# Performance work log

Measured on AMD Instinct MI355X. Metric: run time of the kernel, lower is better.

The kernel has to match this reference:

```python
import jax, jax.numpy as jnp
import numpy as np

B, NUM_IN = 256, 4096
C1, C2 = 64, 128
K1, K2, P1, P2 = 9, 5, 4, 2
POOL1, POOL2 = 4, 4
H = 256            # rnn_hidden_size
H1, H2 = 256, 128  # mlp hidden sizes
EPS = 1e-5


def setup_inputs() -> dict:
    key = jax.random.key(0)
    ks = jax.random.split(key, 24)
    g = lambda k, shp, scale=0.02: (jax.random.normal(k, shp, jnp.float32) * scale)
    return {
        "x": jax.random.normal(ks[0], (B, 1, NUM_IN), jnp.float32),
        "s": jax.random.normal(ks[1], (B, 1), jnp.float32),
        "conv1_w": g(ks[2], (C1, 1, K1), 0.1), "conv1_b": g(ks[3], (C1,)),
        "bn1_g": jnp.ones((C1,), jnp.float32), "bn1_b": jnp.zeros((C1,), jnp.float32),
        "conv2_w": g(ks[4], (C2, C1, K2), 0.05), "conv2_b": g(ks[5], (C2,)),
        "bn2_g": jnp.ones((C2,), jnp.float32), "bn2_b": jnp.zeros((C2,), jnp.float32),
        "lstm_wi0": g(ks[6], (C2, 4 * H), 0.05), "lstm_bi0": g(ks[7], (4 * H,)),
        "lstm_wh0": g(ks[8], (H, 4 * H), 0.05), "lstm_bh0": g(ks[9], (4 * H,)),
        "lstm_wi1": g(ks[10], (H, 4 * H), 0.05), "lstm_bi1": g(ks[11], (4 * H,)),
        "lstm_wh1": g(ks[12], (H, 4 * H), 0.05), "lstm_bh1": g(ks[13], (4 * H,)),
        "w1": g(ks[14], (H + 1, H1), 0.05), "b1": g(ks[15], (H1,)),
        "w2": g(ks[16], (H1, H2), 0.05), "b2": g(ks[17], (H2,)),
        "wp": g(ks[18], (H2, 1), 0.05), "bp": g(ks[19], (1,)),
    }


def _conv1d(x, w, b, stride, pad):
    # x: [B,C,L], w: [O,I,K]
    y = jax.lax.conv_general_dilated(x, w, (stride,), [(pad, pad)],
                                     dimension_numbers=("NCH", "OIH", "NCH"))
    return y + b[None, :, None]


def _avgpool(x, k):
    Bx, Cx, L = x.shape
    return x.reshape(Bx, Cx, L // k, k).mean(axis=-1)


def _bn(x, gamma, beta):
    # training-mode batchnorm over (N, L) per channel, biased variance
    mu = x.mean(axis=(0, 2), keepdims=True)
    var = ((x - mu) ** 2).mean(axis=(0, 2), keepdims=True)
    xh = (x - mu) * jax.lax.rsqrt(var + EPS)
    return xh * gamma[None, :, None] + beta[None, :, None]


def _lstm_cell(xt, h, c, wi, bi, wh, bh):
    gates = xt @ wi + bi + h @ wh + bh
    i, f, g, o = jnp.split(gates, 4, axis=-1)
    c_new = jax.nn.sigmoid(f) * c + jax.nn.sigmoid(i) * jnp.tanh(g)
    h_new = jax.nn.sigmoid(o) * jnp.tanh(c_new)
    return h_new, c_new


def reference(x, s, conv1_w, conv1_b, bn1_g, bn1_b, conv2_w, conv2_b, bn2_g, bn2_b,
              lstm_wi0, lstm_bi0, lstm_wh0, lstm_bh0,
              lstm_wi1, lstm_bi1, lstm_wh1, lstm_bh1,
              w1, b1, w2, b2, wp, bp):
    x = _bn(_avgpool(jax.nn.relu(_conv1d(x, conv1_w, conv1_b, 1, P1)), POOL1), bn1_g, bn1_b)
    x = _bn(_avgpool(jax.nn.relu(_conv1d(x, conv2_w, conv2_b, 1, P2)), POOL2), bn2_g, bn2_b)
    seq = jnp.transpose(x, (0, 2, 1))          # [B, T, C2]
    seq_t = jnp.transpose(seq, (1, 0, 2))      # [T, B, C2]
    Bx = seq.shape[0]
    init = (jnp.zeros((Bx, H), x.dtype), jnp.zeros((Bx, H), x.dtype),
            jnp.zeros((Bx, H), x.dtype), jnp.zeros((Bx, H), x.dtype))

    def step(carry, xt):
        h0, c0, h1, c1 = carry
        h0, c0 = _lstm_cell(xt, h0, c0, lstm_wi0, lstm_bi0, lstm_wh0, lstm_bh0)
        h1, c1 = _lstm_cell(h0, h1, c1, lstm_wi1, lstm_bi1, lstm_wh1, lstm_bh1)
        return (h0, c0, h1, c1), None

    (h0, c0, h1, c1), _ = jax.lax.scan(step, init, seq_t)
    feat = jnp.concatenate([h1, s], axis=1)    # [B, H+1]
    z = jax.nn.relu(feat @ w1 + b1)            # dropout is identity at eval
    z = jax.nn.relu(z @ w2 + b2)
    return jax.nn.softplus(z @ wp + bp)        # [B, 1]
```

## Files before the change

kernel.cpp:

```cpp
#include <hip/hip_runtime.h>
#include <hip/hip_bf16.h>
#include <hip/hip_fp16.h>
#include <math.h>

#define EPSV 1e-5f

typedef short short8 __attribute__((ext_vector_type(8)));
typedef float f32x4 __attribute__((ext_vector_type(4)));
typedef unsigned long long u64;

#define MFMA(a, b, c) __builtin_amdgcn_mfma_f32_16x16x32_f16(a, b, c, 0, 0, 0)

#define OFF_SC1    8192
#define OFF_SH1    8448
#define OFF_SC2    8704
#define OFF_SH2    9216
#define OFF_B0     9728
#define OFF_B1     13824
#define OFF_PART1  17920
#define OFF_PART2  148992
#define OFF_W2F    411136
#define OFF_WF     493056
#define OFF_SEQ    2328064
#define OFF_H0W    19105280
#define OFF_H1W    19629568
#define OFF_HF     20153856

__device__ __forceinline__ unsigned short f2h(float f) {
  return __half_as_ushort(__float2half(f));
}
__device__ __forceinline__ float h2f(unsigned short u) {
  return __half2float(__ushort_as_half(u));
}
__device__ __forceinline__ float sigf(float x) { return 1.f / (1.f + __expf(-x)); }
__device__ __forceinline__ float tanhfast(float x) {
  return 1.f - 2.f / (__expf(2.f * x) + 1.f);
}

__global__ void k_init(u64* hz) {
  hz[blockIdx.x * 256 + threadIdx.x] = 0ULL;
}

__global__ __launch_bounds__(256, 2) void k_conv1(const float* __restrict__ x,
                                                  const float* __restrict__ w1,
                                                  const float* __restrict__ b1,
                                                  float* __restrict__ part1) {
  __shared__ float xs[4104];
  __shared__ float w1s[576];
  __shared__ float b1s[64];
  __shared__ float red[64][4][2];
  const int tid = threadIdx.x, b = blockIdx.x;
  for (int j = tid; j < 4104; j += 256) {
    int p = j - 4;
    xs[j] = (p >= 0 && p < 4096) ? x[b * 4096 + p] : 0.f;
  }
  for (int j = tid; j < 576; j += 256) w1s[j] = w1[j];
  if (tid < 64) b1s[tid] = b1[tid];
  __syncthreads();
  const int c = tid >> 2, lq = tid & 3;
  float wr[9];
#pragma unroll
  for (int k = 0; k < 9; k++) wr[k] = w1s[c * 9 + k];
  const float bb = b1s[c];
  float S = 0.f, SS = 0.f;
  for (int li = 0; li < 256; li++) {
    int l = lq * 256 + li;
    int base = 4 * l;
    float a4 = 0.f;
#pragma unroll
    for (int jj = 0; jj < 4; jj++) {
      float cv = bb;
#pragma unroll
      for (int k = 0; k < 9; k++) cv += xs[base + jj + k] * wr[k];
      a4 += fmaxf(cv, 0.f);
    }
    float y = 0.25f * a4;
    S += y;
    SS += y * y;
  }
  red[c][lq][0] = S;
  red[c][lq][1] = SS;
  __syncthreads();
  if (tid < 64) {
    float s = 0.f, ss = 0.f;
#pragma unroll
    for (int q = 0; q < 4; q++) {
      s += red[tid][q][0];
      ss += red[tid][q][1];
    }
    part1[(b * 64 + tid) * 2 + 0] = s;
    part1[(b * 64 + tid) * 2 + 1] = ss;
  }
}

__global__ void k_bn1(const float* __restrict__ part1, const float* __restrict__ g,
                      const float* __restrict__ bt, float* __restrict__ sc,
                      float* __restrict__ sh) {
  __shared__ float rs[256], rss[256];
  const int c = blockIdx.x, tid = threadIdx.x;
  rs[tid] = part1[(tid * 64 + c) * 2 + 0];
  rss[tid] = part1[(tid * 64 + c) * 2 + 1];
  __syncthreads();
  for (int st = 128; st > 0; st >>= 1) {
    if (tid < st) {
      rs[tid] += rs[tid + st];
      rss[tid] += rss[tid + st];
    }
    __syncthreads();
  }
  if (tid == 0) {
    const float N = 256.f * 1024.f;
    float mean = rs[0] / N;
    float var = rss[0] / N - mean * mean;
    float scale = g[c] * rsqrtf(var + EPSV);
    sc[c] = scale;
    sh[c] = bt[c] - mean * scale;
  }
}

__global__ void k_w2frag(const float* __restrict__ w2,
                         unsigned short* __restrict__ w2f) {
  int n = blockIdx.x * 256 + threadIdx.x;
  if (n >= 40960) return;
  int e = n & 7, lane = (n >> 3) & 63, ot = (n >> 9) & 7, sc = n >> 12;
  int s = sc >> 1, c2 = sc & 1;
  int o = ot * 16 + (lane & 15);
  int i = c2 * 32 + ((lane >> 4) << 3) + e;
  w2f[n] = f2h(w2[o * 320 + i * 5 + s]);
}

__global__ __launch_bounds__(256, 1) void k_conv2(
    const float* __restrict__ x, const float* __restrict__ w1,
    const float* __restrict__ b1, const float* __restrict__ sc1,
    const float* __restrict__ sh1, const unsigned short* __restrict__ w2f,
    const float* __restrict__ b2, unsigned short* __restrict__ seq,
    float* __restrict__ part2) {
  __shared__ float xs[4104];
  __shared__ unsigned short y1t[1028][66];
  __shared__ float w1s[576], b1s[64], s1s[64], h1s[64], b2s[128];
  __shared__ float red[4][2][128];
  const int tid = threadIdx.x, b = blockIdx.x;
  for (int j = tid; j < 4104; j += 256) {
    int p = j - 4;
    xs[j] = (p >= 0 && p < 4096) ? x[b * 4096 + p] : 0.f;
  }
  for (int j = tid; j < 576; j += 256) w1s[j] = w1[j];
  if (tid < 64) {
    b1s[tid] = b1[tid];
    s1s[tid] = sc1[tid];
    h1s[tid] = sh1[tid];
  }
  if (tid < 128) b2s[tid] = b2[tid];
  if (tid < 132) {
    int r4 = tid / 33, c4 = tid % 33;
    int row = (r4 < 2) ? r4 : (1024 + r4);
    ((unsigned int*)&y1t[row][0])[c4] = 0u;
  }
  __syncthreads();
  {
    const int i2 = tid & 31, lg = tid >> 5;
    const int ia = 2 * i2, ib = ia + 1;
    float wra[9], wrb[9];
#pragma unroll
    for (int k = 0; k < 9; k++) {
      wra[k] = w1s[ia * 9 + k];
      wrb[k] = w1s[ib * 9 + k];
    }
    const float bia = b1s[ia], bib = b1s[ib];
    const float sa = s1s[ia], sb = s1s[ib], ha = h1s[ia], hb = h1s[ib];
    for (int j = 0; j < 128; j++) {
      int l = lg * 128 + j;
      float xv[12];
#pragma unroll
      for (int m = 0; m < 12; m++) xv[m] = xs[4 * l + m];
      float aa = 0.f, ab = 0.f;
#pragma unroll
      for (int jj = 0; jj < 4; jj++) {
        float ca = bia, cb = bib;
#pragma unroll
        for (int k = 0; k < 9; k++) {
          float xx = xv[jj + k];
          ca += xx * wra[k];
          cb += xx * wrb[k];
        }
        aa += fmaxf(ca, 0.f);
        ab += fmaxf(cb, 0.f);
      }
      float va = 0.25f * aa * sa + ha;
      float vb = 0.25f * ab * sb + hb;
      unsigned int pk = (unsigned int)f2h(va) | ((unsigned int)f2h(vb) << 16);
      *(unsigned int*)&y1t[l + 2][ia] = pk;
    }
  }
  __syncthreads();
  const int wv = tid >> 6, lane = tid & 63;
  const int colo = lane & 15, rq = lane >> 4;
  float Sa[2][4], SSa[2][4];
#pragma unroll
  for (int a = 0; a < 2; a++)
#pragma unroll
    for (int c = 0; c < 4; c++) {
      Sa[a][c] = 0.f;
      SSa[a][c] = 0.f;
    }
#pragma unroll
  for (int og = 0; og < 2; og++) {
    short8 bf[4][10];
#pragma unroll
    for (int ot = 0; ot < 4; ot++)
#pragma unroll
      for (int sc = 0; sc < 10; sc++)
        bf[ot][sc] = *(const short8*)(w2f + ((sc * 8 + og * 4 + ot) * 64 + lane) * 8);
    for (int ltw = 0; ltw < 16; ltw++) {
      int lt = wv * 16 + ltw;
      int lbase = lt * 16;
      short8 af[10];
#pragma unroll
      for (int s = 0; s < 5; s++)
#pragma unroll
        for (int c2 = 0; c2 < 2; c2++)
          af[s * 2 + c2] =
              *(const short8*)&y1t[lbase + colo + s][c2 * 32 + rq * 8];
#pragma unroll
      for (int ot = 0; ot < 4; ot++) {
        f32x4 acc = {0.f, 0.f, 0.f, 0.f};
#pragma unroll
        for (int sc = 0; sc < 10; sc++)
          acc = MFMA(af[sc], bf[ot][sc], acc);
        int o = (og * 4 + ot) * 16 + colo;
        float bv = b2s[o];
        float s4 = fmaxf(acc[0] + bv, 0.f) + fmaxf(acc[1] + bv, 0.f) +
                   fmaxf(acc[2] + bv, 0.f) + fmaxf(acc[3] + bv, 0.f);
        float y = 0.25f * s4;
        int t_out = lt * 4 + rq;
        seq[(b * 256 + t_out) * 128 + o] = f2h(y);
        Sa[og][ot] += y;
        SSa[og][ot] += y * y;
      }
    }
  }
#pragma unroll
  for (int og = 0; og < 2; og++)
#pragma unroll
    for (int ot = 0; ot < 4; ot++) {
      float sv = Sa[og][ot], ssv = SSa[og][ot];
      sv += __shfl_xor(sv, 16, 64);
      sv += __shfl_xor(sv, 32, 64);
      ssv += __shfl_xor(ssv, 16, 64);
      ssv += __shfl_xor(ssv, 32, 64);
      if (rq == 0) {
        int o = (og * 4 + ot) * 16 + colo;
        red[wv][0][o] = sv;
        red[wv][1][o] = ssv;
      }
    }
  __syncthreads();
  if (tid < 128) {
    float s = red[0][0][tid] + red[1][0][tid] + red[2][0][tid] + red[3][0][tid];
    float ss = red[0][1][tid] + red[1][1][tid] + red[2][1][tid] + red[3][1][tid];
    part2[(b * 128 + tid) * 2 + 0] = s;
    part2[(b * 128 + tid) * 2 + 1] = ss;
  }
}

__global__ void k_bn2(const float* __restrict__ part2, const float* __restrict__ g,
                      const float* __restrict__ bt, float* __restrict__ sc,
                      float* __restrict__ sh) {
  __shared__ float rs[256], rss[256];
  const int o = blockIdx.x, tid = threadIdx.x;
  rs[tid] = part2[(tid * 128 + o) * 2 + 0];
  rss[tid] = part2[(tid * 128 + o) * 2 + 1];
  __syncthreads();
  for (int st = 128; st > 0; st >>= 1) {
    if (tid < st) {
      rs[tid] += rs[tid + st];
      rss[tid] += rss[tid + st];
    }
    __syncthreads();
  }
  if (tid == 0) {
    const float N = 65536.f;
    float mean = rs[0] / N;
    float var = rss[0] / N - mean * mean;
    float scale = g[o] * rsqrtf(var + EPSV);
    sc[o] = scale;
    sh[o] = bt[o] - mean * scale;
  }
}

__global__ void k_bias(const float* __restrict__ bi0, const float* __restrict__ bh0,
                       const float* __restrict__ wi0, const float* __restrict__ sh2,
                       const float* __restrict__ bi1, const float* __restrict__ bh1,
                       float* __restrict__ b0arr, float* __restrict__ b1arr) {
  int g = blockIdx.x * 256 + threadIdx.x;
  float s = bi0[g] + bh0[g];
  for (int k = 0; k < 128; k++) s += sh2[k] * wi0[k * 1024 + g];
  b0arr[g] = s;
  b1arr[g] = bi1[g] + bh1[g];
}

__global__ void k_wfrag(const float* __restrict__ wi0, const float* __restrict__ wh0,
                        const float* __restrict__ wi1, const float* __restrict__ wh1,
                        const float* __restrict__ sc2,
                        unsigned short* __restrict__ wf) {
  const int slot = blockIdx.x / 56;
  const int idx = (blockIdx.x % 56) * 256 + threadIdx.x;
  const int j = idx >> 9, lane = (idx >> 3) & 63, e = idx & 7;
  const int sh = slot >> 2, wv = slot & 3;
  const int m = lane & 15;
  const int gcol = (m & 3) * 256 + sh * 16 + wv * 4 + (m >> 2);
  float v;
  if (j < 12) {
    int k = j * 32 + ((lane >> 4) << 3) + e;
    v = (k < 128) ? sc2[k] * wi0[k * 1024 + gcol] : wh0[(k - 128) * 1024 + gcol];
  } else {
    int k = (j - 12) * 32 + ((lane >> 4) << 3) + e;
    v = (k < 256) ? wi1[k * 1024 + gcol] : wh1[(k - 256) * 1024 + gcol];
  }
  wf[slot * 14336 + idx] = f2h(v);
}

__global__ __launch_bounds__(256, 1) void k_lstm(
    const unsigned short* __restrict__ seq, const unsigned short* __restrict__ wf,
    const float* __restrict__ b0arr, const float* __restrict__ b1arr,
    u64* __restrict__ h0w, u64* __restrict__ h1w, float* __restrict__ hfinal) {
  __shared__ unsigned short wlds[4 * 28 * 64 * 8];
  __shared__ unsigned short hs0[2][16 * 264];
  __shared__ unsigned short hs1[2][16 * 264];
  const int tid = threadIdx.x;
  const int gb = blockIdx.x >> 4, sh = blockIdx.x & 15;
  const int b0 = gb * 16;
  const int wv = tid >> 6, lane = tid & 63;
  const int bt = lane & 15;
  const int ul = lane >> 4;
  const int q8 = ul * 8;

  {
    const u64* src = (const u64*)(wf + sh * 4 * 14336);
    u64* dst = (u64*)wlds;
    for (int j = tid; j < 14336; j += 256) dst[j] = src[j];
  }
#define LW(j) (*(const short8*)&wlds[(((wv)*28 + (j)) * 64 + lane) * 8])

  f32x4 b0v, b1v;
#pragma unroll
  for (int r = 0; r < 4; r++) {
    int gcol = r * 256 + sh * 16 + wv * 4 + ul;
    b0v[r] = b0arr[gcol];
    b1v[r] = b1arr[gcol];
  }
  float c0 = 0.f, c1 = 0.f, h1v = 0.f;
  const int pidx = (sh * 8 + wv * 2 + (ul >> 1)) * 16 + bt;
  u64* const st0base = h0w + gb * 2048 + pidx;
  u64* const st1base = h1w + gb * 2048 + pidx;
  __syncthreads();

  {
    const unsigned short* xp = seq + ((b0 + bt) * 256 + 0) * 128 + q8;
    short8 xa0 = *(const short8*)(xp + 0);
    short8 xa1 = *(const short8*)(xp + 32);
    short8 xa2 = *(const short8*)(xp + 64);
    short8 xa3 = *(const short8*)(xp + 96);
    f32x4 acc = b0v;
    acc = MFMA(LW(0), xa0, acc);
    acc = MFMA(LW(1), xa1, acc);
    acc = MFMA(LW(2), xa2, acc);
    acc = MFMA(LW(3), xa3, acc);
    c0 = sigf(acc[1]) * c0 + sigf(acc[0]) * tanhfast(acc[2]);
    float h0v = sigf(acc[3]) * tanhfast(c0);
    unsigned v0 = f2h(h0v);
    unsigned v1 = __shfl_down(v0, 16, 64);
    if ((ul & 1) == 0) {
      u64 w = 1ULL | ((u64)v0 << 16) | ((u64)v1 << 32);
      __hip_atomic_store(st0base, w, __ATOMIC_RELAXED, __HIP_MEMORY_SCOPE_AGENT);
    }
  }

  for (int t = 0; t < 256; t++) {
    short8 xa0, xa1, xa2, xa3;
    if (t < 255) {
      const unsigned short* xp = seq + ((b0 + bt) * 256 + (t + 1)) * 128 + q8;
      xa0 = *(const short8*)(xp + 0);
      xa1 = *(const short8*)(xp + 32);
      xa2 = *(const short8*)(xp + 64);
      xa3 = *(const short8*)(xp + 96);
    }
    const u64* q0 = h0w + (t & 1) * 32768 + gb * 2048;
    const u64* q1 = h1w + ((t + 1) & 1) * 32768 + gb * 2048;
    const unsigned e0 = (unsigned)(t + 1), e1 = (unsigned)t;
    u64 w0[8], w1[8];
#pragma unroll
    for (int u = 0; u < 8; u++)
      w1[u] = __hip_atomic_load(q1 + u * 256 + tid, __ATOMIC_RELAXED,
                                __HIP_MEMORY_SCOPE_AGENT);
    {
      int spin = 0;
      for (;;) {
        bool ok = true;
#pragma unroll
        for (int u = 0; u < 8; u++)
          w0[u] = __hip_atomic_load(q0 + u * 256 + tid, __ATOMIC_RELAXED,
                                    __HIP_MEMORY_SCOPE_AGENT);
#pragma unroll
        for (int u = 0; u < 8; u++)
          ok = ok & ((unsigned)(unsigned short)w0[u] == e0);
        if (__all(ok)) break;
        if (++spin > 2) __builtin_amdgcn_s_sleep(2);
      }
    }
    {
      bool ok = true;
#pragma unroll
      for (int u = 0; u < 8; u++)
        ok = ok & ((unsigned)(unsigned short)w1[u] == e1);
      while (!__all(ok)) {
        ok = true;
#pragma unroll
        for (int u = 0; u < 8; u++) {
          w1[u] = __hip_atomic_load(q1 + u * 256 + tid, __ATOMIC_RELAXED,
                                    __HIP_MEMORY_SCOPE_AGENT);
          ok = ok & ((unsigned)(unsigned short)w1[u] == e1);
        }
      }
    }
    const int hb = t & 1;
#pragma unroll
    for (int u = 0; u < 8; u++) {
      int g = u * 256 + tid;
      int bw = g & 15, p = g >> 4;
      *(unsigned*)&hs0[hb][bw * 264 + 2 * p] = (unsigned)(w0[u] >> 16);
      *(unsigned*)&hs1[hb][bw * 264 + 2 * p] = (unsigned)(w1[u] >> 16);
    }
    __syncthreads();
    short8 ha[8], hbf[8];
#pragma unroll
    for (int kk = 0; kk < 8; kk++) {
      ha[kk] = *(const short8*)&hs0[hb][bt * 264 + kk * 32 + q8];
      hbf[kk] = *(const short8*)&hs1[hb][bt * 264 + kk * 32 + q8];
    }
    if (t < 255) {
      f32x4 a0a = b0v;
      f32x4 a0b = {0.f, 0.f, 0.f, 0.f};
      a0a = MFMA(LW(0), xa0, a0a);
      a0b = MFMA(LW(1), xa1, a0b);
      a0a = MFMA(LW(2), xa2, a0a);
      a0b = MFMA(LW(3), xa3, a0b);
#pragma unroll
      for (int kk = 0; kk < 8; kk += 2) {
        a0a = MFMA(LW(4 + kk), ha[kk], a0a);
        a0b = MFMA(LW(5 + kk), ha[kk + 1], a0b);
      }
      float gi = a0a[0] + a0b[0], gf = a0a[1] + a0b[1];
      float gg = a0a[2] + a0b[2], go = a0a[3] + a0b[3];
      c0 = sigf(gf) * c0 + sigf(gi) * tanhfast(gg);
      float h0v = sigf(go) * tanhfast(c0);
      unsigned v0 = f2h(h0v);
      unsigned v1 = __shfl_down(v0, 16, 64);
      if ((ul & 1) == 0) {
        u64 w = (u64)(unsigned short)(t + 2) | ((u64)v0 << 16) | ((u64)v1 << 32);
        __hip_atomic_store(st0base + ((t + 1) & 1) * 32768, w, __ATOMIC_RELAXED,
                           __HIP_MEMORY_SCOPE_AGENT);
      }
    }
    {
      f32x4 acc1a = b1v;
      f32x4 acc1b = {0.f, 0.f, 0.f, 0.f};
#pragma unroll
      for (int kk = 0; kk < 8; kk++) {
        acc1a = MFMA(LW(12 + kk), ha[kk], acc1a);
        acc1b = MFMA(LW(20 + kk), hbf[kk], acc1b);
      }
      float gi = acc1a[0] + acc1b[0], gf = acc1a[1] + acc1b[1];
      float gg = acc1a[2] + acc1b[2], go = acc1a[3] + acc1b[3];
      c1 = sigf(gf) * c1 + sigf(gi) * tanhfast(gg);
      h1v = sigf(go) * tanhfast(c1);
      if (t < 255) {
        unsigned v0 = f2h(h1v);
        unsigned v1 = __shfl_down(v0, 16, 64);
        if ((ul & 1) == 0) {
          u64 w = (u64)(unsigned short)(t + 1) | ((u64)v0 << 16) | ((u64)v1 << 32);
          __hip_atomic_store(st1base + (t & 1) * 32768, w, __ATOMIC_RELAXED,
                             __HIP_MEMORY_SCOPE_AGENT);
        }
      }
    }
  }
  hfinal[(b0 + bt) * 256 + sh * 16 + wv * 4 + ul] = h1v;
}

__global__ __launch_bounds__(256, 2) void k_mlp(const float* __restrict__ hfinal,
                                                const float* __restrict__ s,
                                                const float* __restrict__ w1,
                                                const float* __restrict__ b1,
                                                const float* __restrict__ w2,
                                                const float* __restrict__ b2,
                                                const float* __restrict__ wp,
                                                const float* __restrict__ bp,
                                                float* __restrict__ out) {
  __shared__ float feat[257];
  __shared__ float z1[256];
  __shared__ float z2[128];
  const int tid = threadIdx.x, b = blockIdx.x;
  feat[tid] = hfinal[b * 256 + tid];
  if (tid == 0) feat[256] = s[b];
  __syncthreads();
  float a = b1[tid];
  for (int i = 0; i < 257; i++) a += feat[i] * w1[i * 256 + tid];
  z1[tid] = fmaxf(a, 0.f);
  __syncthreads();
  if (tid < 128) {
    float a2 = b2[tid];
    for (int i = 0; i < 256; i++) a2 += z1[i] * w2[i * 128 + tid];
    z2[tid] = fmaxf(a2, 0.f);
  }
  __syncthreads();
  if (tid == 0) {
    float sv = bp[0];
    for (int i = 0; i < 128; i++) sv += z2[i] * wp[i];
    out[b] = fmaxf(sv, 0.f) + log1pf(__expf(-fabsf(sv)));
  }
}

extern "C" void kernel_launch(void* const* d_in, const int* in_sizes, int n_in,
                              void* d_out, int out_size, void* d_ws, size_t ws_size,
                              hipStream_t stream) {
  const float* x = (const float*)d_in[0];
  const float* s = (const float*)d_in[1];
  const float* c1w = (const float*)d_in[2];
  const float* c1b = (const float*)d_in[3];
  const float* bn1g = (const float*)d_in[4];
  const float* bn1b = (const float*)d_in[5];
  const float* c2w = (const float*)d_in[6];
  const float* c2b = (const float*)d_in[7];
  const float* bn2g = (const float*)d_in[8];
  const float* bn2b = (const float*)d_in[9];
  const float* wi0 = (const float*)d_in[10];
  const float* bi0 = (const float*)d_in[11];
  const float* wh0 = (const float*)d_in[12];
  const float* bh0 = (const float*)d_in[13];
  const float* wi1 = (const float*)d_in[14];
  const float* bi1 = (const float*)d_in[15];
  const float* wh1 = (const float*)d_in[16];
  const float* bh1 = (const float*)d_in[17];
  const float* w1 = (const float*)d_in[18];
  const float* b1 = (const float*)d_in[19];
  const float* w2 = (const float*)d_in[20];
  const float* b2 = (const float*)d_in[21];
  const float* wp = (const float*)d_in[22];
  const float* bp = (const float*)d_in[23];

  char* ws = (char*)d_ws;
  float* sc1 = (float*)(ws + OFF_SC1);
  float* sh1 = (float*)(ws + OFF_SH1);
  float* sc2 = (float*)(ws + OFF_SC2);
  float* sh2 = (float*)(ws + OFF_SH2);
  float* b0arr = (float*)(ws + OFF_B0);
  float* b1arr = (float*)(ws + OFF_B1);
  float* part1 = (float*)(ws + OFF_PART1);
  float* part2 = (float*)(ws + OFF_PART2);
  unsigned short* w2f = (unsigned short*)(ws + OFF_W2F);
  unsigned short* wf = (unsigned short*)(ws + OFF_WF);
  unsigned short* seq = (unsigned short*)(ws + OFF_SEQ);
  u64* h0w = (u64*)(ws + OFF_H0W);
  u64* h1w = (u64*)(ws + OFF_H1W);
  float* hf = (float*)(ws + OFF_HF);

  k_init<<<512, 256, 0, stream>>>(h0w);
  k_conv1<<<256, 256, 0, stream>>>(x, c1w, c1b, part1);
  k_bn1<<<64, 256, 0, stream>>>(part1, bn1g, bn1b, sc1, sh1);
  k_w2frag<<<160, 256, 0, stream>>>(c2w, w2f);
  k_conv2<<<256, 256, 0, stream>>>(x, c1w, c1b, sc1, sh1, w2f, c2b, seq, part2);
  k_bn2<<<128, 256, 0, stream>>>(part2, bn2g, bn2b, sc2, sh2);
  k_bias<<<4, 256, 0, stream>>>(bi0, bh0, wi0, sh2, bi1, bh1, b0arr, b1arr);
  k_wfrag<<<3584, 256, 0, stream>>>(wi0, wh0, wi1, wh1, sc2, wf);
  k_lstm<<<256, 256, 0, stream>>>(seq, wf, b0arr, b1arr, h0w, h1w, hf);
  k_mlp<<<256, 256, 0, stream>>>(hf, s, w1, b1, w2, b2, wp, bp, (float*)d_out);
}
```

Measured before the change: 918.1 us.

## Defer layer-1 hidden-state wait until after input-side MFMAs; triple-buffer h1 exchange

The persistent LSTM kernel now waits only for the layer-0 hidden state at the start of each step. It issues the layer-1 input MFMAs on h0 before spinning on the layer-1 recurrent state, so cross-block sync latency overlaps with compute. The h1 exchange buffer goes from double to triple buffering (mod 3 indexing), with the workspace offset and init size enlarged to match. The cost is an extra __syncthreads per step, modulo arithmetic, and removal of the s_sleep backoff in the h0 spin loop, which can raise memory polling pressure.

Result: slower. 965.0 us (+5.1%).

```diff
diff --git a/kernel.cpp b/kernel.cpp
--- a/kernel.cpp
+++ b/kernel.cpp
@@ -24,7 +24,7 @@
 #define OFF_SEQ    2328064
 #define OFF_H0W    19105280
 #define OFF_H1W    19629568
-#define OFF_HF     20153856
+#define OFF_HF     20416000
 
 __device__ __forceinline__ unsigned short f2h(float f) {
   return __half_as_ushort(__float2half(f));
@@ -38,7 +38,8 @@
 }
 
 __global__ void k_init(u64* hz) {
-  hz[blockIdx.x * 256 + threadIdx.x] = 0ULL;
+  int i = blockIdx.x * 256 + threadIdx.x;
+  if (i < 163840) hz[i] = 0ULL;
 }
 
 __global__ __launch_bounds__(256, 2) void k_conv1(const float* __restrict__ x,
@@ -386,42 +387,20 @@
       xa3 = *(const short8*)(xp + 96);
     }
     const u64* q0 = h0w + (t & 1) * 32768 + gb * 2048;
-    const u64* q1 = h1w + ((t + 1) & 1) * 32768 + gb * 2048;
-    const unsigned e0 = (unsigned)(t + 1), e1 = (unsigned)t;
-    u64 w0[8], w1[8];
-#pragma unroll
-    for (int u = 0; u < 8; u++)
-      w1[u] = __hip_atomic_load(q1 + u * 256 + tid, __ATOMIC_RELAXED,
-                                __HIP_MEMORY_SCOPE_AGENT);
-    {
-      int spin = 0;
-      for (;;) {
-        bool ok = true;
-#pragma unroll
-        for (int u = 0; u < 8; u++)
-          w0[u] = __hip_atomic_load(q0 + u * 256 + tid, __ATOMIC_RELAXED,
-                                    __HIP_MEMORY_SCOPE_AGENT);
-#pragma unroll
-        for (int u = 0; u < 8; u++)
-          ok = ok & ((unsigned)(unsigned short)w0[u] == e0);
-        if (__all(ok)) break;
-        if (++spin > 2) __builtin_amdgcn_s_sleep(2);
-      }
-    }
-    {
+    const u64* q1 = h1w + ((t + 2) % 3) * 32768 + gb * 2048;
+    const unsigned e0 = (unsigned)(unsigned short)(t + 1);
+    const unsigned e1 = (unsigned)(unsigned short)t;
+    u64 w0[8];
+    for (;;) {
       bool ok = true;
 #pragma unroll
       for (int u = 0; u < 8; u++)
-        ok = ok & ((unsigned)(unsigned short)w1[u] == e1);
-      while (!__all(ok)) {
-        ok = true;
-#pragma unroll
-        for (int u = 0; u < 8; u++) {
-          w1[u] = __hip_atomic_load(q1 + u * 256 + tid, __ATOMIC_RELAXED,
-                                    __HIP_MEMORY_SCOPE_AGENT);
-          ok = ok & ((unsigned)(unsigned short)w1[u] == e1);
-        }
-      }
+        w0[u] = __hip_atomic_load(q0 + u * 256 + tid, __ATOMIC_RELAXED,
+                                  __HIP_MEMORY_SCOPE_AGENT);
+#pragma unroll
+      for (int u = 0; u < 8; u++)
+        ok = ok & ((unsigned)(unsigned short)w0[u] == e0);
+      if (__all(ok)) break;
     }
     const int hb = t & 1;
 #pragma unroll
@@ -429,15 +408,12 @@
       int g = u * 256 + tid;
       int bw = g & 15, p = g >> 4;
       *(unsigned*)&hs0[hb][bw * 264 + 2 * p] = (unsigned)(w0[u] >> 16);
-      *(unsigned*)&hs1[hb][bw * 264 + 2 * p] = (unsigned)(w1[u] >> 16);
     }
     __syncthreads();
-    short8 ha[8], hbf[8];
-#pragma unroll
-    for (int kk = 0; kk < 8; kk++) {
+    short8 ha[8];
+#pragma unroll
+    for (int kk = 0; kk < 8; kk++)
       ha[kk] = *(const short8*)&hs0[hb][bt * 264 + kk * 32 + q8];
-      hbf[kk] = *(const short8*)&hs1[hb][bt * 264 + kk * 32 + q8];
-    }
     if (t < 255) {
       f32x4 a0a = b0v;
       f32x4 a0b = {0.f, 0.f, 0.f, 0.f};
@@ -462,13 +438,36 @@
                            __HIP_MEMORY_SCOPE_AGENT);
       }
     }
+    f32x4 acc1a = b1v;
+#pragma unroll
+    for (int kk = 0; kk < 8; kk++) acc1a = MFMA(LW(12 + kk), ha[kk], acc1a);
+    u64 w1[8];
     {
-      f32x4 acc1a = b1v;
+      bool ok;
+      do {
+        ok = true;
+#pragma unroll
+        for (int u = 0; u < 8; u++)
+          w1[u] = __hip_atomic_load(q1 + u * 256 + tid, __ATOMIC_RELAXED,
+                                    __HIP_MEMORY_SCOPE_AGENT);
+#pragma unroll
+        for (int u = 0; u < 8; u++)
+          ok = ok & ((unsigned)(unsigned short)w1[u] == e1);
+      } while (!__all(ok));
+    }
+#pragma unroll
+    for (int u = 0; u < 8; u++) {
+      int g = u * 256 + tid;
+      int bw = g & 15, p = g >> 4;
+      *(unsigned*)&hs1[hb][bw * 264 + 2 * p] = (unsigned)(w1[u] >> 16);
+    }
+    __syncthreads();
+    {
       f32x4 acc1b = {0.f, 0.f, 0.f, 0.f};
 #pragma unroll
       for (int kk = 0; kk < 8; kk++) {
-        acc1a = MFMA(LW(12 + kk), ha[kk], acc1a);
-        acc1b = MFMA(LW(20 + kk), hbf[kk], acc1b);
+        short8 hbf = *(const short8*)&hs1[hb][bt * 264 + kk * 32 + q8];
+        acc1b = MFMA(LW(20 + kk), hbf, acc1b);
       }
       float gi = acc1a[0] + acc1b[0], gf = acc1a[1] + acc1b[1];
       float gg = acc1a[2] + acc1b[2], go = acc1a[3] + acc1b[3];
@@ -479,7 +478,7 @@
         unsigned v1 = __shfl_down(v0, 16, 64);
         if ((ul & 1) == 0) {
           u64 w = (u64)(unsigned short)(t + 1) | ((u64)v0 << 16) | ((u64)v1 << 32);
-          __hip_atomic_store(st1base + (t & 1) * 32768, w, __ATOMIC_RELAXED,
+          __hip_atomic_store(st1base + (t % 3) * 32768, w, __ATOMIC_RELAXED,
                              __HIP_MEMORY_SCOPE_AGENT);
         }
       }
@@ -565,7 +564,7 @@
   u64* h1w = (u64*)(ws + OFF_H1W);
   float* hf = (float*)(ws + OFF_HF);
 
-  k_init<<<512, 256, 0, stream>>>(h0w);
+  k_init<<<640, 256, 0, stream>>>(h0w);
   k_conv1<<<256, 256, 0, stream>>>(x, c1w, c1b, part1);
   k_bn1<<<64, 256, 0, stream>>>(part1, bn1g, bn1b, sc1, sh1);
   k_w2frag<<<160, 256, 0, stream>>>(c2w, w2f);
```
